# Optimization experiments

Hardware: AMD Instinct MI355X
Metric: run time of the kernel (lower is better)

## Reference

```python
import jax, jax.numpy as jnp
import numpy as np

HEADS = 16
KV_HEADS = 4
DIM_HEAD = 64
DIM = 1024
B, N = 2, 2048


def setup_inputs() -> dict:
    key = jax.random.key(0)
    k1, k2, k3 = jax.random.split(key, 3)
    x = jax.random.normal(k1, (B, N, DIM), dtype=jnp.float32)
    Wq = jax.random.normal(k2, (DIM, HEADS * DIM_HEAD), dtype=jnp.float32) / np.sqrt(DIM)
    Wkv = jax.random.normal(k3, (DIM, 2 * KV_HEADS * DIM_HEAD), dtype=jnp.float32) / np.sqrt(DIM)
    k_scale = jnp.ones((HEADS, 1, DIM_HEAD), dtype=jnp.float32)
    return {"x": x, "Wq": Wq, "Wkv": Wkv, "k_scale": k_scale}


def reference(x, Wq, Wkv, k_scale):
    b, n, _ = x.shape
    g = HEADS // KV_HEADS  # query heads per kv head
    scale = DIM_HEAD ** -0.5
    # fused qkv projections (no bias)
    q = (x @ Wq).reshape(b, n, HEADS, DIM_HEAD)
    kv = x @ Wkv
    k, v = jnp.split(kv, 2, axis=-1)
    k = k.reshape(b, n, KV_HEADS, DIM_HEAD).transpose(0, 2, 1, 3)  # b k n d
    v = v.reshape(b, n, KV_HEADS, DIM_HEAD).transpose(0, 2, 1, 3)  # b k n d
    # group query heads: b, kv_heads, g, n, d
    qg = q.transpose(0, 2, 1, 3).reshape(b, KV_HEADS, g, n, DIM_HEAD)
    # per-query-head k scale, applied to the group-broadcast k (qk-norm)
    ks = k_scale.reshape(KV_HEADS, g, 1, DIM_HEAD)
    kk = k[:, :, None, :, :] * ks  # b k g n d
    dots = jnp.einsum('bkgid,bkgjd->bkgij', qg, kk) * scale
    attn = jax.nn.softmax(dots, axis=-1)
    out = jnp.einsum('bkgij,bkjd->bkgid', attn, v)  # v broadcast over g
    out = out.reshape(b, HEADS, n, DIM_HEAD).transpose(0, 2, 1, 3).reshape(b, n, HEADS * DIM_HEAD)
    return out
```

## Files before the change

kernel.cpp:

```cpp
#include <hip/hip_runtime.h>
#include <stdint.h>
#include <math.h>

typedef __attribute__((ext_vector_type(8))) __bf16 bf16x8;
typedef __attribute__((ext_vector_type(4))) float f32x4;
typedef __attribute__((ext_vector_type(16))) float f32x16;

__device__ __forceinline__ uint32_t f32_to_bf16_rne(float f) {
  union { float f; uint32_t u; } v; v.f = f;
  return (v.u + 0x7FFFu + ((v.u >> 16) & 1u)) >> 16;
}

__device__ __forceinline__ uint32_t cvt_pk_bf16(float lo, float hi) {
  uint32_t r;
  asm("v_cvt_pk_bf16_f32 %0, %1, %2" : "=v"(r) : "v"(lo), "v"(hi));
  return r;
}

__device__ __forceinline__ void gld16(void* lds, const void* g) {
  __builtin_amdgcn_global_load_lds(
      (__attribute__((address_space(1))) void*)(g),
      (__attribute__((address_space(3))) void*)(lds), 16, 0, 0);
}

__device__ __forceinline__ f32x4 mfma16(bf16x8 a, bf16x8 b, f32x4 c) {
  return __builtin_amdgcn_mfma_f32_16x16x32_bf16(a, b, c, 0, 0, 0);
}
__device__ __forceinline__ f32x16 mfma32(bf16x8 a, bf16x8 b, f32x16 c) {
  return __builtin_amdgcn_mfma_f32_32x32x16_bf16(a, b, c, 0, 0, 0);
}

#define LOG2E 1.44269504088896340736f

__global__ __launch_bounds__(256) void k_convert(const float* __restrict__ x,
                                                 const float* __restrict__ wq,
                                                 const float* __restrict__ wkv,
                                                 uint16_t* __restrict__ xb,
                                                 uint16_t* __restrict__ wt) {
  __shared__ float tile[64][65];
  int blk = blockIdx.x;
  int t = threadIdx.x;
  if (blk < 2048) {
    int i = blk * 256 + t;
    const float4* xv = (const float4*)x;
    float4 a = xv[2 * i], b2 = xv[2 * i + 1];
    uint32_t w0 = f32_to_bf16_rne(a.x) | (f32_to_bf16_rne(a.y) << 16);
    uint32_t w1 = f32_to_bf16_rne(a.z) | (f32_to_bf16_rne(a.w) << 16);
    uint32_t w2 = f32_to_bf16_rne(b2.x) | (f32_to_bf16_rne(b2.y) << 16);
    uint32_t w3 = f32_to_bf16_rne(b2.z) | (f32_to_bf16_rne(b2.w) << 16);
    ((uint4*)xb)[i] = make_uint4(w0, w1, w2, w3);
  } else {
    int blk2 = blk - 2048;
    int c0 = (blk2 % 24) * 64, k0 = (blk2 / 24) * 64;
    int col = t & 63, rq = t >> 6;
#pragma unroll
    for (int rr = 0; rr < 16; rr++) {
      int r = rr * 4 + rq;
      int c = c0 + col;
      float v = (c < 1024) ? wq[(uint64_t)(k0 + r) * 1024 + c]
                           : wkv[(uint64_t)(k0 + r) * 512 + (c - 1024)];
      tile[r][col] = v;
    }
    __syncthreads();
#pragma unroll
    for (int rr = 0; rr < 16; rr++) {
      int a = rr * 4 + rq;
      wt[(uint64_t)(c0 + a) * 1024 + k0 + col] = (uint16_t)f32_to_bf16_rne(tile[col][a]);
    }
  }
}

__global__ __launch_bounds__(256, 3) void k_proj_gemm(
    const uint16_t* __restrict__ xb, const uint16_t* __restrict__ wt,
    const float* __restrict__ kscale, uint16_t* __restrict__ q_ws,
    uint16_t* __restrict__ kf_ws, uint16_t* __restrict__ vf_ws) {
  __shared__ __align__(16) uint16_t ring[4][6144];
  int t = threadIdx.x;
  int w = t >> 6, l = t & 63;
  int lq = l & 15, lg = l >> 4;
  int m0 = blockIdx.x * 128, n0 = blockIdx.y * 64;
  int wr = w >> 1, wc = w & 1;
  f32x4 acc[4][2] = {};

  auto stage = [&](int slot, int k0) {
#pragma unroll
    for (int j = 0; j < 2; j++) {
      int tt = j * 256 + t;
      int r = tt >> 2, s = tt & 3;
      int sl = s ^ ((r >> 1) & 3);
      gld16((char*)&ring[slot][0] + (j * 256 + w * 64) * 16,
            xb + (uint64_t)(m0 + r) * 1024 + k0 + sl * 8);
    }
    {
      int r = t >> 2, s = t & 3;
      int sl = s ^ ((r >> 1) & 3);
      gld16((char*)&ring[slot][4096] + (w * 64) * 16,
            wt + (uint64_t)(n0 + r) * 1024 + k0 + sl * 8);
    }
  };

  struct PFrags { bf16x8 a[4]; bf16x8 b[2]; };
  auto readFrags = [&](PFrags& F, int slot) {
    const uint16_t* As = &ring[slot][0];
    const uint16_t* Bs = &ring[slot][4096];
#pragma unroll
    for (int m = 0; m < 4; m++) {
      int r = wr * 64 + m * 16 + lq;
      int s = lg ^ ((r >> 1) & 3);
      F.a[m] = *(const bf16x8*)(As + r * 32 + s * 8);
    }
#pragma unroll
    for (int n = 0; n < 2; n++) {
      int r = wc * 32 + n * 16 + lq;
      int s = lg ^ ((r >> 1) & 3);
      F.b[n] = *(const bf16x8*)(Bs + r * 32 + s * 8);
    }
  };

  auto pbody = [&](int tt2, PFrags& C, PFrags& N) {
    int kn = (tt2 + 3) * 32;
    if (kn > 992) kn = 992;
    stage((tt2 + 3) & 3, kn);
    __builtin_amdgcn_s_setprio(1);
#pragma unroll
    for (int m = 0; m < 4; m++)
#pragma unroll
      for (int n = 0; n < 2; n++)
        acc[m][n] = mfma16(C.a[m], C.b[n], acc[m][n]);
    __builtin_amdgcn_s_setprio(0);
    int tn = tt2 + 1;
    if (tn > 31) tn = 31;
    readFrags(N, tn & 3);
    asm volatile("s_waitcnt vmcnt(3) lgkmcnt(0)" ::: "memory");
    __builtin_amdgcn_s_barrier();
  };

  stage(0, 0);
  stage(1, 32);
  stage(2, 64);
  asm volatile("s_waitcnt vmcnt(3)" ::: "memory");
  __builtin_amdgcn_s_barrier();
  PFrags FA, FB;
  readFrags(FA, 0);
  for (int sp = 0; sp < 16; ++sp) {
    pbody(2 * sp, FA, FB);
    pbody(2 * sp + 1, FB, FA);
  }

#pragma unroll
  for (int m = 0; m < 4; m++)
#pragma unroll
    for (int n = 0; n < 2; n++)
#pragma unroll
      for (int jj = 0; jj < 4; jj++) {
        int row = m0 + wr * 64 + m * 16 + 4 * lg + jj;
        int col = n0 + wc * 32 + n * 16 + lq;
        float val = acc[m][n][jj];
        int b = row >> 11, nn = row & 2047;
        if (col < 1024) {
          val *= kscale[col] * 0.125f * LOG2E;
          q_ws[((uint64_t)((b * 16 + (col >> 6)) * 2048 + nn)) * 64 + (col & 63)] =
              (uint16_t)f32_to_bf16_rne(val);
        } else if (col < 1280) {
          int kvh = (col - 1024) >> 6;
          int d = col & 63;
          int gsu = nn >> 5, lrr = nn & 31;
          int mm = d >> 4, hh = (d >> 3) & 1, el = d & 7;
          kf_ws[(uint64_t)(b * 4 + kvh) * 131072 +
                (uint64_t)((((gsu * 4 + mm) * 64) + hh * 32 + lrr) * 8 + el)] =
              (uint16_t)f32_to_bf16_rne(val);
        } else {
          int kvh = (col - 1280) >> 6;
          int d = col & 63;
          int gsu = nn >> 5, jj2 = (nn >> 4) & 1, hh = (nn >> 3) & 1, el = nn & 7;
          int dd = d >> 5, lrr = d & 31;
          vf_ws[(uint64_t)(b * 4 + kvh) * 131072 +
                (uint64_t)((((gsu * 4 + dd * 2 + jj2) * 64) + hh * 32 + lrr) * 8 + el)] =
              (uint16_t)f32_to_bf16_rne(val);
        }
      }
}

__global__ __launch_bounds__(512, 4) void k_attn(const uint16_t* __restrict__ q_ws,
                                                 const uint16_t* __restrict__ kf_ws,
                                                 const uint16_t* __restrict__ vf_ws,
                                                 float* __restrict__ out) {
  __shared__ __align__(16) char smem[65536];

  int t = threadIdx.x, w = t >> 6, l = t & 63;
  int lr = l & 31, hi = l >> 5;
  int wq = w & 3, half = w >> 2;
  int blk = blockIdx.x;
  int c = blk & 7, j = blk >> 3;
  int b = c >> 2, kvh = c & 3;
  int h = kvh * 4 + (j >> 4), qb = j & 15;

  const uint16_t* Qb = q_ws + (uint64_t)(b * 16 + h) * 2048 * 64;
  const uint16_t* Kb = kf_ws + (uint64_t)(b * 4 + kvh) * 131072;
  const uint16_t* Vb = vf_ws + (uint64_t)(b * 4 + kvh) * 131072;
  int qrow0 = qb * 128 + wq * 32;

  bf16x8 qfrag[4];
#pragma unroll
  for (int m = 0; m < 4; m++)
    qfrag[m] = *(const bf16x8*)(Qb + (uint64_t)(qrow0 + lr) * 64 + m * 16 + hi * 8);

  f32x16 oacc[2] = {};
  float l_run = 0.f;

  const uint16_t* Sb = (wq < 2) ? Kb : Vb;
  auto stage = [&](int slot, int sul) {
    int gsu = half * 32 + sul;
    char* dst = smem + slot * 16384 + half * 8192 + wq * 2048 + l * 16;
    const uint16_t* src = Sb + (uint64_t)(gsu * 4 + (wq & 1) * 2) * 512 + l * 8;
    gld16(dst, src);
    gld16(dst + 1024, src + 512);
  };

  auto slotbase = [&](int slot) {
    return (const uint16_t*)(smem + slot * 16384 + half * 8192);
  };

  auto finish = [&](f32x16& Tc, const uint16_t* baseC) {
    float p[16];
#pragma unroll
    for (int e = 0; e < 16; e++) p[e] = __builtin_amdgcn_exp2f(Tc[e]);
    float sm0 = ((p[0] + p[1]) + (p[2] + p[3])) + ((p[4] + p[5]) + (p[6] + p[7]));
    float sm1 = ((p[8] + p[9]) + (p[10] + p[11])) + ((p[12] + p[13]) + (p[14] + p[15]));
    l_run += sm0 + sm1;

    bf16x8 pa[2];
#pragma unroll
    for (int jj = 0; jj < 2; jj++) {
      const float* pp = p + 8 * jj;
      uint32_t X = cvt_pk_bf16(pp[0], pp[1]);
      uint32_t Z = cvt_pk_bf16(pp[2], pp[3]);
      uint32_t Y = cvt_pk_bf16(pp[4], pp[5]);
      uint32_t W2 = cvt_pk_bf16(pp[6], pp[7]);
      asm volatile("v_permlane32_swap_b32 %0, %1" : "+v"(X), "+v"(Y));
      asm volatile("v_permlane32_swap_b32 %0, %1" : "+v"(Z), "+v"(W2));
      union { uint32_t u[4]; bf16x8 v; } pu;
      pu.u[0] = X; pu.u[1] = Z; pu.u[2] = Y; pu.u[3] = W2;
      pa[jj] = pu.v;
    }

    bf16x8 vf[4];
#pragma unroll
    for (int i = 0; i < 4; i++) vf[i] = *(const bf16x8*)(baseC + (4 + i) * 512 + l * 8);
    __builtin_amdgcn_s_setprio(1);
#pragma unroll
    for (int dd = 0; dd < 2; dd++)
#pragma unroll
      for (int jj = 0; jj < 2; jj++)
        oacc[dd] = mfma32(pa[jj], vf[dd * 2 + jj], oacc[dd]);
    __builtin_amdgcn_s_setprio(0);
  };

  auto body = [&](int su, f32x16& Tc, f32x16& Tn) {
    int sn = su + 3;
    if (sn > 31) sn = 31;
    stage((su + 3) & 3, sn);
    const uint16_t* baseN = slotbase((su + 1) & 3);
    bf16x8 kf[4];
#pragma unroll
    for (int m = 0; m < 4; m++) kf[m] = *(const bf16x8*)(baseN + m * 512 + l * 8);
    Tn = (f32x16){};
    __builtin_amdgcn_s_setprio(1);
#pragma unroll
    for (int m = 0; m < 4; m++) Tn = mfma32(kf[m], qfrag[m], Tn);
    __builtin_amdgcn_s_setprio(0);
    finish(Tc, slotbase(su & 3));
    asm volatile("s_waitcnt vmcnt(2) lgkmcnt(0)" ::: "memory");
    __builtin_amdgcn_s_barrier();
  };

  stage(0, 0);
  stage(1, 1);
  stage(2, 2);
  asm volatile("s_waitcnt vmcnt(2)" ::: "memory");
  __builtin_amdgcn_s_barrier();

  f32x16 TA = {}, TB = {};
  {
    const uint16_t* b0 = slotbase(0);
    bf16x8 kf0[4];
#pragma unroll
    for (int m = 0; m < 4; m++) kf0[m] = *(const bf16x8*)(b0 + m * 512 + l * 8);
#pragma unroll
    for (int m = 0; m < 4; m++) TA = mfma32(kf0[m], qfrag[m], TA);
  }
  for (int sp = 0; sp < 15; ++sp) {
    body(2 * sp, TA, TB);
    body(2 * sp + 1, TB, TA);
  }
  body(30, TA, TB);
  finish(TB, slotbase(3));

  l_run += __shfl_xor(l_run, 32);

  asm volatile("s_waitcnt vmcnt(0)" ::: "memory");
  __syncthreads();

  float* exch = (float*)smem;
  float* exl = (float*)(smem + 32768);
  if (half == 1) {
#pragma unroll
    for (int r = 0; r < 16; r++) {
      int qr = (r & 3) + 8 * (r >> 2) + 4 * hi;
      exch[wq * 2048 + qr * 64 + lr] = oacc[0][r];
      exch[wq * 2048 + qr * 64 + 32 + lr] = oacc[1][r];
    }
    if (hi == 0) exl[wq * 32 + lr] = l_run;
  }
  __syncthreads();
  if (half == 0) {
    l_run += exl[wq * 32 + lr];
    float inv = 1.0f / l_run;
#pragma unroll
    for (int r = 0; r < 16; r++) {
      int qr = (r & 3) + 8 * (r >> 2) + 4 * hi;
      float iv = __shfl(inv, qr);
      float o0 = oacc[0][r] + exch[wq * 2048 + qr * 64 + lr];
      float o1 = oacc[1][r] + exch[wq * 2048 + qr * 64 + 32 + lr];
      float* orow = out + (uint64_t)(b * 2048 + qrow0 + qr) * 1024 + h * 64 + lr;
      orow[0] = o0 * iv;
      orow[32] = o1 * iv;
    }
  }
}

extern "C" void kernel_launch(void* const* d_in, const int* in_sizes, int n_in,
                              void* d_out, int out_size, void* d_ws, size_t ws_size,
                              hipStream_t stream) {
  const float* x = (const float*)d_in[0];
  const float* wq = (const float*)d_in[1];
  const float* wkv = (const float*)d_in[2];
  const float* kscale = (const float*)d_in[3];
  float* out = (float*)d_out;
  char* ws = (char*)d_ws;
  uint16_t* xb = (uint16_t*)(ws);
  uint16_t* wt = (uint16_t*)(ws + (8ull << 20));
  uint16_t* q_ws = (uint16_t*)(ws + (11ull << 20));
  uint16_t* kf_ws = (uint16_t*)(ws + (19ull << 20));
  uint16_t* vf_ws = (uint16_t*)(ws + (21ull << 20));

  k_convert<<<2432, 256, 0, stream>>>(x, wq, wkv, xb, wt);
  k_proj_gemm<<<dim3(32, 24), 256, 0, stream>>>(xb, wt, kscale, q_ws, kf_ws, vf_ws);
  k_attn<<<512, 512, 0, stream>>>(q_ws, kf_ws, vf_ws, out);
}
```

Before: 78.94 us.

## Double attention block to 256 query rows with 16 waves and deeper K/V ring

The attention kernel now uses 1024-thread blocks, each covering 256 query rows instead of 128. This halves the number of blocks and the total K/V tile traffic per block set. The LDS ring grows to 8 slots (128 KB of dynamic shared memory), staged 6 tiles ahead. Each loop iteration processes two key tiles per barrier, removing the previous skewed QK/PV software pipeline. The trade-off is one block per CU, lower occupancy and larger barrier groups, with less overlap between the QK MFMAs and the softmax/PV work.

```diff
diff --git a/kernel.cpp b/kernel.cpp
--- a/kernel.cpp
+++ b/kernel.cpp
@@ -181,24 +181,24 @@
       }
 }
 
-__global__ __launch_bounds__(512, 4) void k_attn(const uint16_t* __restrict__ q_ws,
-                                                 const uint16_t* __restrict__ kf_ws,
-                                                 const uint16_t* __restrict__ vf_ws,
-                                                 float* __restrict__ out) {
-  __shared__ __align__(16) char smem[65536];
+__global__ __launch_bounds__(1024, 1) void k_attn(const uint16_t* __restrict__ q_ws,
+                                                  const uint16_t* __restrict__ kf_ws,
+                                                  const uint16_t* __restrict__ vf_ws,
+                                                  float* __restrict__ out) {
+  extern __shared__ __align__(16) char smem[];
 
   int t = threadIdx.x, w = t >> 6, l = t & 63;
   int lr = l & 31, hi = l >> 5;
-  int wq = w & 3, half = w >> 2;
+  int wq = w & 7, half = w >> 3;
   int blk = blockIdx.x;
   int c = blk & 7, j = blk >> 3;
   int b = c >> 2, kvh = c & 3;
-  int h = kvh * 4 + (j >> 4), qb = j & 15;
+  int h = kvh * 4 + (j >> 3), qb = j & 7;
 
   const uint16_t* Qb = q_ws + (uint64_t)(b * 16 + h) * 2048 * 64;
   const uint16_t* Kb = kf_ws + (uint64_t)(b * 4 + kvh) * 131072;
   const uint16_t* Vb = vf_ws + (uint64_t)(b * 4 + kvh) * 131072;
-  int qrow0 = qb * 128 + wq * 32;
+  int qrow0 = qb * 256 + wq * 32;
 
   bf16x8 qfrag[4];
 #pragma unroll
@@ -208,15 +208,11 @@
   f32x16 oacc[2] = {};
   float l_run = 0.f;
 
-  const uint16_t* Sb = (wq < 2) ? Kb : Vb;
-  auto stage = [&](int slot, int sul) {
-    int gsu = half * 32 + sul;
-    char* dst = smem + slot * 16384 + half * 8192 + wq * 2048 + l * 16;
-    const uint16_t* src = Sb + (uint64_t)(gsu * 4 + (wq & 1) * 2) * 512 + l * 8;
-    gld16(dst, src);
-    gld16(dst + 1024, src + 512);
-  };
-
+  const uint16_t* SbW = (((w & 7) < 4) ? Kb : Vb) + (uint64_t)half * 65536 +
+                        (uint64_t)(w & 3) * 512 + l * 8;
+  char* dstW = smem + w * 1024 + l * 16;
+
+  auto stage = [&](int slot, int sul) { gld16(dstW + slot * 16384, SbW + sul * 2048); };
   auto slotbase = [&](int slot) {
     return (const uint16_t*)(smem + slot * 16384 + half * 8192);
   };
@@ -256,45 +252,42 @@
     __builtin_amdgcn_s_setprio(0);
   };
 
-  auto body = [&](int su, f32x16& Tc, f32x16& Tn) {
-    int sn = su + 3;
-    if (sn > 31) sn = 31;
-    stage((su + 3) & 3, sn);
-    const uint16_t* baseN = slotbase((su + 1) & 3);
-    bf16x8 kf[4];
-#pragma unroll
-    for (int m = 0; m < 4; m++) kf[m] = *(const bf16x8*)(baseN + m * 512 + l * 8);
-    Tn = (f32x16){};
+#pragma unroll
+  for (int tt = 0; tt < 6; ++tt) stage(tt, tt);
+  asm volatile("s_waitcnt vmcnt(4)" ::: "memory");
+  __builtin_amdgcn_s_barrier();
+
+  for (int iv = 0; iv < 16; ++iv) {
+    int a = 2 * iv;
+    int s0 = a + 6, s1 = a + 7;
+    if (s0 > 31) s0 = 31;
+    if (s1 > 31) s1 = 31;
+    stage((a + 6) & 7, s0);
+    stage((a + 7) & 7, s1);
+
+    const uint16_t* baseA = slotbase(a & 7);
+    const uint16_t* baseB = slotbase((a + 1) & 7);
+
+    bf16x8 kfA[4], kfB[4];
+#pragma unroll
+    for (int m = 0; m < 4; m++) kfA[m] = *(const bf16x8*)(baseA + m * 512 + l * 8);
+#pragma unroll
+    for (int m = 0; m < 4; m++) kfB[m] = *(const bf16x8*)(baseB + m * 512 + l * 8);
+
+    f32x16 Ta = {}, Tb = {};
     __builtin_amdgcn_s_setprio(1);
 #pragma unroll
-    for (int m = 0; m < 4; m++) Tn = mfma32(kf[m], qfrag[m], Tn);
+    for (int m = 0; m < 4; m++) Ta = mfma32(kfA[m], qfrag[m], Ta);
+#pragma unroll
+    for (int m = 0; m < 4; m++) Tb = mfma32(kfB[m], qfrag[m], Tb);
     __builtin_amdgcn_s_setprio(0);
-    finish(Tc, slotbase(su & 3));
-    asm volatile("s_waitcnt vmcnt(2) lgkmcnt(0)" ::: "memory");
+
+    finish(Ta, baseA);
+    finish(Tb, baseB);
+
+    asm volatile("s_waitcnt vmcnt(4)" ::: "memory");
     __builtin_amdgcn_s_barrier();
-  };
-
-  stage(0, 0);
-  stage(1, 1);
-  stage(2, 2);
-  asm volatile("s_waitcnt vmcnt(2)" ::: "memory");
-  __builtin_amdgcn_s_barrier();
-
-  f32x16 TA = {}, TB = {};
-  {
-    const uint16_t* b0 = slotbase(0);
-    bf16x8 kf0[4];
-#pragma unroll
-    for (int m = 0; m < 4; m++) kf0[m] = *(const bf16x8*)(b0 + m * 512 + l * 8);
-#pragma unroll
-    for (int m = 0; m < 4; m++) TA = mfma32(kf0[m], qfrag[m], TA);
-  }
-  for (int sp = 0; sp < 15; ++sp) {
-    body(2 * sp, TA, TB);
-    body(2 * sp + 1, TB, TA);
-  }
-  body(30, TA, TB);
-  finish(TB, slotbase(3));
+  }
 
   l_run += __shfl_xor(l_run, 32);
 
@@ -302,7 +295,7 @@
   __syncthreads();
 
   float* exch = (float*)smem;
-  float* exl = (float*)(smem + 32768);
+  float* exl = (float*)(smem + 65536);
   if (half == 1) {
 #pragma unroll
     for (int r = 0; r < 16; r++) {
@@ -344,7 +337,14 @@
   uint16_t* kf_ws = (uint16_t*)(ws + (19ull << 20));
   uint16_t* vf_ws = (uint16_t*)(ws + (21ull << 20));
 
+  static bool attr_set = false;
+  if (!attr_set) {
+    (void)hipFuncSetAttribute((const void*)k_attn,
+                              hipFuncAttributeMaxDynamicSharedMemorySize, 131072);
+    attr_set = true;
+  }
+
   k_convert<<<2432, 256, 0, stream>>>(x, wq, wkv, xb, wt);
   k_proj_gemm<<<dim3(32, 24), 256, 0, stream>>>(xb, wt, kscale, q_ws, kf_ws, vf_ws);
-  k_attn<<<512, 512, 0, stream>>>(q_ws, kf_ws, vf_ws, out);
-}
+  k_attn<<<256, 1024, 131072, stream>>>(q_ws, kf_ws, vf_ws, out);
+}
```

Measured after the change: 77.45 us. About the same (-1.9%).
